# Kernel optimization log

Hardware: AMD Instinct MI355X
Metric: run time of the kernel (lower is better)

The kernel has to match this reference:

```python
import jax, jax.numpy as jnp
import numpy as np

POOLING_COUNTS = [15, 8, 8]
N_CLIPS = 64


def build_mask_and_indices(pooling_counts, N):
    """Replicates the static index construction in __init__ (pure numpy)."""
    mask2d = np.zeros((N, N), dtype=bool)
    mask2d[np.arange(N), np.arange(N)] = True
    maskij = []
    pool_specs = []  # (kernel, stride) for each level
    for gi, c in enumerate(pooling_counts):
        if gi == 0:
            pool_specs.extend([(2, 1)] * c)
        else:
            pool_specs.extend([(3, 2)] + [(2, 1)] * (c - 1))
    stride, offset = 1, 0
    for c in pooling_counts:
        for _ in range(c):
            offset += stride
            i = np.arange(0, N - offset, stride)
            j = np.arange(offset, N, stride)
            mask2d[i, j] = True
            maskij.append((i, j))
        stride *= 2
    return mask2d, maskij, pool_specs


def maxpool1d(x, k, s):
    # x: [B, D, L]; MaxPool1d(kernel=k, stride=s), no padding
    L = x.shape[-1]
    out_len = (L - k) // s + 1
    idx = np.arange(out_len)[:, None] * s + np.arange(k)[None, :]  # [out_len, k]
    return x[..., idx].max(axis=-1)


def setup_inputs() -> dict:
    key = jax.random.key(0)
    x = jax.random.normal(key, (16, 512, N_CLIPS), dtype=jnp.float32)
    return {"x": x}


def reference(x):
    B, D, N = x.shape
    mask2d_np, maskij, pool_specs = build_mask_and_indices(POOLING_COUNTS, N)
    diag = np.arange(N)

    # diagonal scatter: map2d[:, :, n, n] = x[:, :, n]
    base = jnp.zeros((B, D, N, N), dtype=x.dtype).at[:, :, diag, diag].set(x)

    # boundary map: average of endpoint features at each (i, j) line
    boundary_map2d = base
    for i, j in maskij:
        boundary_map2d = boundary_map2d.at[:, :, i, j].set((x[:, :, i] + x[:, :, j]) * 0.5)

    # content map: pyramid of max-pools scattered onto the same lines
    content_map2d = base
    xp = x
    for (k, s), (i, j) in zip(pool_specs, maskij):
        xp = maxpool1d(xp, k, s)
        content_map2d = content_map2d.at[:, :, i, j].set(xp)

    mask2d = jnp.broadcast_to(jnp.asarray(mask2d_np)[None, None], (B, 1, N, N))
    return boundary_map2d, content_map2d, mask2d
```

## Files before the change

### kernel.cpp

```cpp
#include <hip/hip_runtime.h>


#define T_PER_WAVE 2

__global__ __launch_bounds__(256) void sbc_kernel(const float* __restrict__ x,
                                                  float* __restrict__ out,
                                                  size_t mapsz) {
    const int lane = threadIdx.x & 63;
    const int wid  = blockIdx.x * 4 + (threadIdx.x >> 6);
    const int j    = lane;

    const int sh = 63 - j;
    const unsigned long long mbits =
          (1ULL << j)
        | (0x7FFF000000000000ULL >> sh)
        | ((0x0000555500000000ULL >> sh) & 0x5555555555555555ULL)
        | ((0x0000000011111111ULL >> sh) & 0x1111111111111111ULL);

    const int tile0 = wid * T_PER_WAVE;

    float xv[T_PER_WAVE];
#pragma unroll
    for (int tt = 0; tt < T_PER_WAVE; ++tt)
        xv[tt] = x[(size_t)(tile0 + tt) * 64 + j];

#pragma unroll
    for (int tt = 0; tt < T_PER_WAVE; ++tt) {
        const int tile = tile0 + tt;
        float* __restrict__ bout = out + (size_t)tile * 4096;
        float* __restrict__ cout = bout + mapsz;
        const float xj = xv[tt];
        float r = xj;
#pragma unroll
        for (int i = 63; i >= 0; --i) {
            const float xi = __shfl(xv[tt], i, 64);
            const float xs = (j >= i) ? xi : -INFINITY;
            r = fmaxf(r, xs);
            const bool on  = (mbits >> i) & 1ULL;
            const float s  = on ? 0.5f : 0.0f;
            const float s2 = on ? 1.0f : 0.0f;
            bout[i * 64 + j] = s * (xi + xj);
            cout[i * 64 + j] = s2 * r;
        }
        if ((tile & 511) == 0) {
            float* __restrict__ mout = out + 2 * mapsz + (size_t)(tile >> 9) * 4096;
#pragma unroll
            for (int i = 0; i < 64; ++i)
                mout[i * 64 + j] = ((mbits >> i) & 1ULL) ? 1.0f : 0.0f;
        }
    }
}

extern "C" void kernel_launch(void* const* d_in, const int* in_sizes, int n_in,
                              void* d_out, int out_size, void* d_ws, size_t ws_size,
                              hipStream_t stream) {
    const float* x = (const float*)d_in[0];
    float* out = (float*)d_out;
    const int N  = 64;
    const int BD = in_sizes[0] / N;
    const size_t mapsz = (size_t)BD * N * N;
    const int nwaves = BD / T_PER_WAVE;
    sbc_kernel<<<dim3(nwaves / 4), dim3(256), 0, stream>>>(x, out, mapsz);
}
```

Baseline: 250.4 us.

## Vectorize output stores to float4 with nontemporal writes, 4 tiles per wave

```diff
diff --git a/kernel.cpp b/kernel.cpp
--- a/kernel.cpp
+++ b/kernel.cpp
@@ -1,52 +1,77 @@
 #include <hip/hip_runtime.h>
 
 
-#define T_PER_WAVE 2
+typedef float f32x4 __attribute__((ext_vector_type(4)));
 
 __global__ __launch_bounds__(256) void sbc_kernel(const float* __restrict__ x,
                                                   float* __restrict__ out,
                                                   size_t mapsz) {
     const int lane = threadIdx.x & 63;
     const int wid  = blockIdx.x * 4 + (threadIdx.x >> 6);
-    const int j    = lane;
+    const int g    = lane >> 4;
+    const int t    = lane & 15;
+    const int j0   = t * 4;
+    const int tile = wid * 4 + g;
 
-    const int sh = 63 - j;
-    const unsigned long long mbits =
-          (1ULL << j)
-        | (0x7FFF000000000000ULL >> sh)
-        | ((0x0000555500000000ULL >> sh) & 0x5555555555555555ULL)
-        | ((0x0000000011111111ULL >> sh) & 0x1111111111111111ULL);
+    const float* xt = x + (size_t)tile * 64;
 
-    const int tile0 = wid * T_PER_WAVE;
+    float xall[64];
+#pragma unroll
+    for (int k = 0; k < 16; ++k) {
+        f32x4 v = *(const f32x4*)(xt + 4 * k);
+        xall[4 * k + 0] = v[0];
+        xall[4 * k + 1] = v[1];
+        xall[4 * k + 2] = v[2];
+        xall[4 * k + 3] = v[3];
+    }
+    const f32x4 xj = *(const f32x4*)(xt + j0);
 
-    float xv[T_PER_WAVE];
+    unsigned long long mb[4];
 #pragma unroll
-    for (int tt = 0; tt < T_PER_WAVE; ++tt)
-        xv[tt] = x[(size_t)(tile0 + tt) * 64 + j];
+    for (int c = 0; c < 4; ++c) {
+        const int j  = j0 + c;
+        const int sh = 63 - j;
+        mb[c] = (1ULL << j)
+              | (0x7FFF000000000000ULL >> sh)
+              | ((0x0000555500000000ULL >> sh) & 0x5555555555555555ULL)
+              | ((0x0000000011111111ULL >> sh) & 0x1111111111111111ULL);
+    }
+
+    const f32x4 xj05 = xj * 0.5f;
+    float r[4];
+#pragma unroll
+    for (int c = 0; c < 4; ++c) r[c] = xj[c];
+
+    float* __restrict__ bout = out + (size_t)tile * 4096 + j0;
+    float* __restrict__ cout = bout + mapsz;
 
 #pragma unroll
-    for (int tt = 0; tt < T_PER_WAVE; ++tt) {
-        const int tile = tile0 + tt;
-        float* __restrict__ bout = out + (size_t)tile * 4096;
-        float* __restrict__ cout = bout + mapsz;
-        const float xj = xv[tt];
-        float r = xj;
+    for (int i = 63; i >= 0; --i) {
+        const float xi   = xall[i];
+        const float xi05 = xi * 0.5f;
+        f32x4 bv, cv;
 #pragma unroll
-        for (int i = 63; i >= 0; --i) {
-            const float xi = __shfl(xv[tt], i, 64);
+        for (int c = 0; c < 4; ++c) {
+            const int j = j0 + c;
             const float xs = (j >= i) ? xi : -INFINITY;
-            r = fmaxf(r, xs);
-            const bool on  = (mbits >> i) & 1ULL;
-            const float s  = on ? 0.5f : 0.0f;
-            const float s2 = on ? 1.0f : 0.0f;
-            bout[i * 64 + j] = s * (xi + xj);
-            cout[i * 64 + j] = s2 * r;
+            r[c] = fmaxf(r[c], xs);
+            const bool on = (mb[c] >> i) & 1ULL;
+            bv[c] = on ? (xi05 + xj05[c]) : 0.0f;
+            cv[c] = on ? r[c] : 0.0f;
         }
-        if ((tile & 511) == 0) {
-            float* __restrict__ mout = out + 2 * mapsz + (size_t)(tile >> 9) * 4096;
+        __builtin_nontemporal_store(bv, (f32x4*)(bout + i * 64));
+        __builtin_nontemporal_store(cv, (f32x4*)(cout + i * 64));
+    }
+
+    if (g == 0 && (wid & 127) == 0) {
+        float* __restrict__ mout = out + 2 * mapsz + (size_t)(wid >> 7) * 4096 + j0;
 #pragma unroll
-            for (int i = 0; i < 64; ++i)
-                mout[i * 64 + j] = ((mbits >> i) & 1ULL) ? 1.0f : 0.0f;
+        for (int i = 0; i < 64; ++i) {
+            f32x4 mv;
+#pragma unroll
+            for (int c = 0; c < 4; ++c)
+                mv[c] = ((mb[c] >> i) & 1ULL) ? 1.0f : 0.0f;
+            __builtin_nontemporal_store(mv, (f32x4*)(mout + i * 64));
         }
     }
 }
@@ -59,6 +84,6 @@
     const int N  = 64;
     const int BD = in_sizes[0] / N;
     const size_t mapsz = (size_t)BD * N * N;
-    const int nwaves = BD / T_PER_WAVE;
+    const int nwaves = BD / 4;
     sbc_kernel<<<dim3(nwaves / 4), dim3(256), 0, stream>>>(x, out, mapsz);
 }
```

Measured after the change: 266.7 us. 6.5% more time.
